# Kernel tuning notes

Hardware: AMD Instinct MI355X
Metric: run time of the kernel (lower is better)

## Reference

```python
import jax, jax.numpy as jnp
import numpy as np

B, N, D, H = 256, 256, 136, 128  # queries, docs/query, feature dim, hidden dim


def setup_inputs() -> dict:
    key = jax.random.key(0)
    ks = jax.random.split(key, 7)
    features = jax.random.uniform(ks[0], (B, N, D), dtype=jnp.float32)
    labels = jax.random.randint(ks[1], (B, N), 0, 5, dtype=jnp.int32)  # relevance grades 0..4
    # Small init scales keep MLP scores in (-1, 1) so log2(1 + max(s_i, s_j)) is well-defined
    W1 = jax.random.normal(ks[2], (D, H), dtype=jnp.float32) * 0.05
    b1 = jnp.zeros((H,), dtype=jnp.float32)
    W2 = jax.random.normal(ks[3], (H, H), dtype=jnp.float32) * 0.05
    b2 = jnp.zeros((H,), dtype=jnp.float32)
    W3 = jax.random.normal(ks[4], (H, 1), dtype=jnp.float32) * 0.02
    b3 = jnp.zeros((1,), dtype=jnp.float32)
    return {"features": features, "labels": labels,
            "W1": W1, "b1": b1, "W2": W2, "b2": b2, "W3": W3, "b3": b3}


def _scores(features, W1, b1, W2, b2, W3, b3):
    # Linear-ReLU-(Dropout: identity in eval)-Linear-ReLU-Linear, then squeeze(-1)
    h = jax.nn.relu(jnp.einsum('bnd,dh->bnh', features, W1) + b1)
    h = jax.nn.relu(jnp.einsum('bnh,hk->bnk', h, W2) + b2)
    return (jnp.einsum('bnh,ho->bno', h, W3) + b3).squeeze(-1)  # [B, N]


def _compute_lambdas(scores, labels):
    si = scores[:, :, None]        # s_i  [B, N, 1]
    sj = scores[:, None, :]        # s_j  [B, 1, N]
    li = labels[:, :, None]
    lj = labels[:, None, :]
    # lambda_ij = 0.5 * (1 - sigmoid(s_j - s_i)) = 0.5 * sigmoid(s_i - s_j)
    lam = 0.5 * jax.nn.sigmoid(si - sj)
    gain = jnp.exp2(labels.astype(scores.dtype))  # 2 ** l
    dndcg = jnp.abs((gain[:, :, None] - gain[:, None, :])
                    / (1.0 + jnp.log2(1.0 + jnp.maximum(si, sj))))
    A = jnp.where(li > lj, lam * dndcg, jnp.zeros((), scores.dtype))  # [B, N, N]
    # lambdas[i] += A[i, j] over j (pairs where l_i > l_j); lambdas[j] -= A[i, j]
    return A.sum(-1) - A.sum(-2)  # [B, N]


def reference(features, labels, W1, b1, W2, b2, W3, b3):
    scores = _scores(features, W1, b1, W2, b2, W3, b3)
    return _compute_lambdas(scores, labels)
```

## Files before the change

### kernel.cpp

```cpp
#include <hip/hip_runtime.h>
#include <hip/hip_bf16.h>

#define DIN  136
#define HH   128
#define NSEQ 256
#define NB   256
#define K1P  168

typedef __attribute__((ext_vector_type(4))) float f32x4;
typedef __attribute__((ext_vector_type(2))) float f32x2;
typedef __attribute__((ext_vector_type(8))) short bf16x8;

static __device__ __forceinline__ unsigned short f2bf(float f) {
    unsigned int u = __float_as_uint(f);
    u += 0x7fffu + ((u >> 16) & 1u);
    return (unsigned short)(u >> 16);
}

__global__ __launch_bounds__(256)
void prep_kernel(const float* __restrict__ W1, const float* __restrict__ W2,
                 short* __restrict__ w1t, short* __restrict__ w2t)
{
    const int nt = gridDim.x * 256;
    const int idx = blockIdx.x * 256 + threadIdx.x;
    for (int e = idx; e < HH * K1P; e += nt) {
        const int n = e / K1P, k = e - n * K1P;
        w1t[e] = (k < DIN) ? (short)f2bf(W1[k * HH + n]) : (short)0;
    }
    for (int e = idx; e < HH * HH; e += nt) {
        const int n = e >> 7, k = e & 127;
        w2t[e] = (short)f2bf(W2[k * HH + n]);
    }
}

__global__ __launch_bounds__(1024, 4)
void fused_kernel(const float* __restrict__ features,
                  const int*   __restrict__ labels,
                  const short* __restrict__ w1t,
                  const short* __restrict__ w2t,
                  const float* __restrict__ b1, const float* __restrict__ b2,
                  const float* __restrict__ W3, const float* __restrict__ b3,
                  float* __restrict__ out)
{
    __shared__ short  a_lds[NSEQ * K1P];
    __shared__ float4 sp[NSEQ];
    __shared__ float  s_part[4][NSEQ];

    const int t    = threadIdx.x;
    const int lane = t & 63;
    const int wv   = t >> 6;
    const int l15  = lane & 15;
    const int l4   = lane >> 4;
    const long row0 = (long)blockIdx.x * NSEQ;

    {
        const f32x2* src = (const f32x2*)(features + row0 * DIN);
        for (int i = t; i < NSEQ * DIN / 2; i += 1024) {
            f32x2 v = src[i];
            const int e = i * 2;
            const int r = e / DIN, k = e - r * DIN;
            *(unsigned int*)&a_lds[r * K1P + k] =
                (unsigned int)f2bf(v.x) | ((unsigned int)f2bf(v.y) << 16);
        }
        for (int i = t; i < NSEQ * 16; i += 1024) {
            const int r = i >> 4, k = DIN + (i & 15) * 2;
            *(unsigned int*)&a_lds[r * K1P + k] = 0u;
        }
    }
    __syncthreads();

    const int arow = (wv * 16 + l15) * K1P;

    f32x4 acc[8];
#pragma unroll
    for (int tn = 0; tn < 8; ++tn) {
        const float bv = b1[tn * 16 + l15];
        acc[tn] = (f32x4){bv, bv, bv, bv};
    }
    for (int kc = 0; kc < 5; ++kc) {
        const int kb = kc * 32 + l4 * 8;
        const bf16x8 afr = *(const bf16x8*)&a_lds[arow + kb];
        bf16x8 bfr[8];
#pragma unroll
        for (int tn = 0; tn < 8; ++tn)
            bfr[tn] = *(const bf16x8*)&w1t[(tn * 16 + l15) * K1P + kb];
#pragma unroll
        for (int tn = 0; tn < 8; ++tn)
            acc[tn] = __builtin_amdgcn_mfma_f32_16x16x32_bf16(afr, bfr[tn], acc[tn], 0, 0, 0);
    }

#pragma unroll
    for (int tn = 0; tn < 8; ++tn) {
        const int col = tn * 16 + l15;
#pragma unroll
        for (int j = 0; j < 4; ++j)
            a_lds[(wv * 16 + l4 * 4 + j) * K1P + col] =
                (short)f2bf(fmaxf(acc[tn][j], 0.f));
    }

    f32x4 acc2[8];
#pragma unroll
    for (int tn = 0; tn < 8; ++tn) {
        const float bv = b2[tn * 16 + l15];
        acc2[tn] = (f32x4){bv, bv, bv, bv};
    }
    for (int kc = 0; kc < 4; ++kc) {
        const int kb = kc * 32 + l4 * 8;
        const bf16x8 afr = *(const bf16x8*)&a_lds[arow + kb];
        bf16x8 bfr[8];
#pragma unroll
        for (int tn = 0; tn < 8; ++tn)
            bfr[tn] = *(const bf16x8*)&w2t[(tn * 16 + l15) * HH + kb];
#pragma unroll
        for (int tn = 0; tn < 8; ++tn)
            acc2[tn] = __builtin_amdgcn_mfma_f32_16x16x32_bf16(afr, bfr[tn], acc2[tn], 0, 0, 0);
    }

    {
        float w3v[8];
#pragma unroll
        for (int tn = 0; tn < 8; ++tn) w3v[tn] = W3[tn * 16 + l15];
        const float b3v = b3[0];
#pragma unroll
        for (int j = 0; j < 4; ++j) {
            float p = 0.f;
#pragma unroll
            for (int tn = 0; tn < 8; ++tn)
                p += fmaxf(acc2[tn][j], 0.f) * w3v[tn];
            p += __shfl_xor(p, 1, 64);
            p += __shfl_xor(p, 2, 64);
            p += __shfl_xor(p, 4, 64);
            p += __shfl_xor(p, 8, 64);
            if (l15 == 0) {
                const int row = wv * 16 + l4 * 4 + j;
                const float s = p + b3v;
                const int lab = labels[row0 + row];
                const float g = 0.5f * exp2f((float)lab);
                const float disc = 1.f / (1.f + log2f(1.f + s));
                sp[row] = make_float4(s * 1.44269504088896f,
                                      g, disc, 0.f);
            }
        }
    }
    __syncthreads();

    {
        const int i  = t & (NSEQ - 1);
        const int jg = t >> 8;
        const float4 me = sp[i];
        const float sci = me.x, gi = me.y, di = me.z;
        float accum = 0.f;
        const int j0 = jg * 64;
#pragma unroll 8
        for (int jj = 0; jj < 64; ++jj) {
            const float4 o = sp[j0 + jj];
            const float dg = o.y - gi;
            const float e  = exp2f(o.x - sci);
            const float r  = __builtin_amdgcn_rcpf(1.f + e);
            const float dmax = (sci > o.x) ? di : o.z;
            const float dn = fabsf(dg) * dmax;
            const float w  = (dg < 0.f) ? r : (r - 1.f);
            accum += dn * w;
        }
        s_part[jg][i] = accum;
    }
    __syncthreads();
    {
        const int i  = t & (NSEQ - 1);
        if ((t >> 8) == 0)
            out[row0 + i] = s_part[0][i] + s_part[1][i] +
                            s_part[2][i] + s_part[3][i];
    }
}

extern "C" void kernel_launch(void* const* d_in, const int* in_sizes, int n_in,
                              void* d_out, int out_size, void* d_ws, size_t ws_size,
                              hipStream_t stream)
{
    const float* features = (const float*)d_in[0];
    const int*   labels   = (const int*)d_in[1];
    const float* W1 = (const float*)d_in[2];
    const float* b1 = (const float*)d_in[3];
    const float* W2 = (const float*)d_in[4];
    const float* b2 = (const float*)d_in[5];
    const float* W3 = (const float*)d_in[6];
    const float* b3 = (const float*)d_in[7];

    short* w1t = (short*)d_ws;
    short* w2t = w1t + HH * K1P;
    float* out = (float*)d_out;

    prep_kernel<<<64, 256, 0, stream>>>(W1, W2, w1t, w2t);
    fused_kernel<<<NB, 1024, 0, stream>>>(
        features, labels, w1t, w2t, b1, b2, W3, b3, out);
}
```

Measured before the change: 121.8 us.

## Load features directly into MFMA A-fragments, shrink LDS, split B loads

Removes the LDS staging pass for the feature matrix: each lane now reads its fp32 feature row straight from global memory, converts it to bf16 and zeroes the padded K chunk in registers. The LDS buffer shrinks to a 136-stride hidden buffer that holds only layer-1 activations, and the launch bounds now ask for up to 8 waves per SIMD. The weight fragment loads are split into two halves of four to lower register pressure. In exchange, global reads become strided per row with less coalescing, and the row stride of 136 shorts may cause LDS bank conflicts.

```diff
diff --git a/kernel.cpp b/kernel.cpp
--- a/kernel.cpp
+++ b/kernel.cpp
@@ -6,9 +6,9 @@
 #define NSEQ 256
 #define NB   256
 #define K1P  168
+#define S2   136
 
 typedef __attribute__((ext_vector_type(4))) float f32x4;
-typedef __attribute__((ext_vector_type(2))) float f32x2;
 typedef __attribute__((ext_vector_type(8))) short bf16x8;
 
 static __device__ __forceinline__ unsigned short f2bf(float f) {
@@ -33,7 +33,7 @@
     }
 }
 
-__global__ __launch_bounds__(1024, 4)
+__global__ __launch_bounds__(1024, 8)
 void fused_kernel(const float* __restrict__ features,
                   const int*   __restrict__ labels,
                   const short* __restrict__ w1t,
@@ -42,7 +42,7 @@
                   const float* __restrict__ W3, const float* __restrict__ b3,
                   float* __restrict__ out)
 {
-    __shared__ short  a_lds[NSEQ * K1P];
+    __shared__ short  h1[NSEQ * S2];
     __shared__ float4 sp[NSEQ];
     __shared__ float  s_part[4][NSEQ];
 
@@ -53,23 +53,8 @@
     const int l4   = lane >> 4;
     const long row0 = (long)blockIdx.x * NSEQ;
 
-    {
-        const f32x2* src = (const f32x2*)(features + row0 * DIN);
-        for (int i = t; i < NSEQ * DIN / 2; i += 1024) {
-            f32x2 v = src[i];
-            const int e = i * 2;
-            const int r = e / DIN, k = e - r * DIN;
-            *(unsigned int*)&a_lds[r * K1P + k] =
-                (unsigned int)f2bf(v.x) | ((unsigned int)f2bf(v.y) << 16);
-        }
-        for (int i = t; i < NSEQ * 16; i += 1024) {
-            const int r = i >> 4, k = DIN + (i & 15) * 2;
-            *(unsigned int*)&a_lds[r * K1P + k] = 0u;
-        }
-    }
-    __syncthreads();
-
-    const int arow = (wv * 16 + l15) * K1P;
+    const float* frow = features + (row0 + wv * 16 + l15) * (long)DIN;
+    const int    arow = (wv * 16 + l15) * S2;
 
     f32x4 acc[8];
 #pragma unroll
@@ -79,14 +64,30 @@
     }
     for (int kc = 0; kc < 5; ++kc) {
         const int kb = kc * 32 + l4 * 8;
-        const bf16x8 afr = *(const bf16x8*)&a_lds[arow + kb];
-        bf16x8 bfr[8];
-#pragma unroll
-        for (int tn = 0; tn < 8; ++tn)
+        bf16x8 afr;
+        if (kb < DIN) {
+            const f32x4 g0 = *(const f32x4*)&frow[kb];
+            const f32x4 g1 = *(const f32x4*)&frow[kb + 4];
+            afr[0] = (short)f2bf(g0.x); afr[1] = (short)f2bf(g0.y);
+            afr[2] = (short)f2bf(g0.z); afr[3] = (short)f2bf(g0.w);
+            afr[4] = (short)f2bf(g1.x); afr[5] = (short)f2bf(g1.y);
+            afr[6] = (short)f2bf(g1.z); afr[7] = (short)f2bf(g1.w);
+        } else {
+            afr = (bf16x8){0,0,0,0,0,0,0,0};
+        }
+        bf16x8 bfr[4];
+#pragma unroll
+        for (int tn = 0; tn < 4; ++tn)
             bfr[tn] = *(const bf16x8*)&w1t[(tn * 16 + l15) * K1P + kb];
 #pragma unroll
-        for (int tn = 0; tn < 8; ++tn)
+        for (int tn = 0; tn < 4; ++tn)
             acc[tn] = __builtin_amdgcn_mfma_f32_16x16x32_bf16(afr, bfr[tn], acc[tn], 0, 0, 0);
+#pragma unroll
+        for (int tn = 0; tn < 4; ++tn)
+            bfr[tn] = *(const bf16x8*)&w1t[((tn + 4) * 16 + l15) * K1P + kb];
+#pragma unroll
+        for (int tn = 0; tn < 4; ++tn)
+            acc[tn + 4] = __builtin_amdgcn_mfma_f32_16x16x32_bf16(afr, bfr[tn], acc[tn + 4], 0, 0, 0);
     }
 
 #pragma unroll
@@ -94,7 +95,7 @@
         const int col = tn * 16 + l15;
 #pragma unroll
         for (int j = 0; j < 4; ++j)
-            a_lds[(wv * 16 + l4 * 4 + j) * K1P + col] =
+            h1[(wv * 16 + l4 * 4 + j) * S2 + col] =
                 (short)f2bf(fmaxf(acc[tn][j], 0.f));
     }
 
@@ -106,14 +107,20 @@
     }
     for (int kc = 0; kc < 4; ++kc) {
         const int kb = kc * 32 + l4 * 8;
-        const bf16x8 afr = *(const bf16x8*)&a_lds[arow + kb];
-        bf16x8 bfr[8];
-#pragma unroll
-        for (int tn = 0; tn < 8; ++tn)
+        const bf16x8 afr = *(const bf16x8*)&h1[arow + kb];
+        bf16x8 bfr[4];
+#pragma unroll
+        for (int tn = 0; tn < 4; ++tn)
             bfr[tn] = *(const bf16x8*)&w2t[(tn * 16 + l15) * HH + kb];
 #pragma unroll
-        for (int tn = 0; tn < 8; ++tn)
+        for (int tn = 0; tn < 4; ++tn)
             acc2[tn] = __builtin_amdgcn_mfma_f32_16x16x32_bf16(afr, bfr[tn], acc2[tn], 0, 0, 0);
+#pragma unroll
+        for (int tn = 0; tn < 4; ++tn)
+            bfr[tn] = *(const bf16x8*)&w2t[((tn + 4) * 16 + l15) * HH + kb];
+#pragma unroll
+        for (int tn = 0; tn < 4; ++tn)
+            acc2[tn + 4] = __builtin_amdgcn_mfma_f32_16x16x32_bf16(afr, bfr[tn], acc2[tn + 4], 0, 0, 0);
     }
 
     {
@@ -166,7 +173,7 @@
     }
     __syncthreads();
     {
-        const int i  = t & (NSEQ - 1);
+        const int i = t & (NSEQ - 1);
         if ((t >> 8) == 0)
             out[row0 + i] = s_part[0][i] + s_part[1][i] +
                             s_part[2][i] + s_part[3][i];
```

Measured after the change: 125.5 us. 1.03x slower.

## Stage bf16 weights in LDS, shrink row stride, vectorize feature conversion

Applied to the files above, without the earlier changes.

Both bf16 weight matrices are now copied into shared memory once per block and the MFMA B-fragments are read from there instead of from global memory. The row stride drops from 168 to 136, which removes the zero-padding writes. The tail K chunk (128..135) becomes a masked MFMA where only lanes with l4==0 load data. Feature loads are widened to float4 and packed with hardware bf16x2 conversion. LDS use grows to about 136KB with aliased regions, so an extra barrier is added, and occupancy is limited to one block per CU.

```diff
diff --git a/kernel.cpp b/kernel.cpp
--- a/kernel.cpp
+++ b/kernel.cpp
@@ -5,46 +5,51 @@
 #define HH   128
 #define NSEQ 256
 #define NB   256
-#define K1P  168
+#define ST   136
 
 typedef __attribute__((ext_vector_type(4))) float f32x4;
-typedef __attribute__((ext_vector_type(2))) float f32x2;
 typedef __attribute__((ext_vector_type(8))) short bf16x8;
 
-static __device__ __forceinline__ unsigned short f2bf(float f) {
-    unsigned int u = __float_as_uint(f);
-    u += 0x7fffu + ((u >> 16) & 1u);
-    return (unsigned short)(u >> 16);
+static __device__ __forceinline__ unsigned cvt2(float lo, float hi) {
+    __hip_bfloat162 h = __float22bfloat162_rn(make_float2(lo, hi));
+    return *(unsigned*)&h;
+}
+static __device__ __forceinline__ short f2bf1(float f) {
+    __hip_bfloat16 h = __float2bfloat16(f);
+    return *(short*)&h;
 }
 
 __global__ __launch_bounds__(256)
 void prep_kernel(const float* __restrict__ W1, const float* __restrict__ W2,
-                 short* __restrict__ w1t, short* __restrict__ w2t)
+                 short* __restrict__ w1s, short* __restrict__ w2s)
 {
     const int nt = gridDim.x * 256;
     const int idx = blockIdx.x * 256 + threadIdx.x;
-    for (int e = idx; e < HH * K1P; e += nt) {
-        const int n = e / K1P, k = e - n * K1P;
-        w1t[e] = (k < DIN) ? (short)f2bf(W1[k * HH + n]) : (short)0;
-    }
-    for (int e = idx; e < HH * HH; e += nt) {
-        const int n = e >> 7, k = e & 127;
-        w2t[e] = (short)f2bf(W2[k * HH + n]);
+    for (int e = idx; e < HH * ST; e += nt) {
+        const int n = e / ST, k = e - n * ST;
+        w1s[e] = f2bf1(W1[k * HH + n]);
+    }
+    for (int e = idx; e < HH * ST; e += nt) {
+        const int n = e / ST, k = e - n * ST;
+        w2s[e] = (k < HH) ? f2bf1(W2[k * HH + n]) : (short)0;
     }
 }
 
 __global__ __launch_bounds__(1024, 4)
 void fused_kernel(const float* __restrict__ features,
                   const int*   __restrict__ labels,
-                  const short* __restrict__ w1t,
-                  const short* __restrict__ w2t,
+                  const short* __restrict__ w1s,
+                  const short* __restrict__ w2s,
                   const float* __restrict__ b1, const float* __restrict__ b2,
                   const float* __restrict__ W3, const float* __restrict__ b3,
                   float* __restrict__ out)
 {
-    __shared__ short  a_lds[NSEQ * K1P];
-    __shared__ float4 sp[NSEQ];
-    __shared__ float  s_part[4][NSEQ];
+    __shared__ __align__(16) char smem[139264];
+    short* a_lds  = (short*)smem;
+    short* w1_lds = (short*)(smem + 69632);
+    short* w2_lds = (short*)(smem + 104448);
+    float4* sp    = (float4*)smem;
+    float (*s_part)[NSEQ] = (float (*)[NSEQ])(smem + 4096);
 
     const int t    = threadIdx.x;
     const int lane = t & 63;
@@ -54,55 +59,31 @@
     const long row0 = (long)blockIdx.x * NSEQ;
 
     {
-        const f32x2* src = (const f32x2*)(features + row0 * DIN);
-        for (int i = t; i < NSEQ * DIN / 2; i += 1024) {
-            f32x2 v = src[i];
-            const int e = i * 2;
-            const int r = e / DIN, k = e - r * DIN;
-            *(unsigned int*)&a_lds[r * K1P + k] =
-                (unsigned int)f2bf(v.x) | ((unsigned int)f2bf(v.y) << 16);
-        }
-        for (int i = t; i < NSEQ * 16; i += 1024) {
-            const int r = i >> 4, k = DIN + (i & 15) * 2;
-            *(unsigned int*)&a_lds[r * K1P + k] = 0u;
-        }
-    }
-    __syncthreads();
-
-    const int arow = (wv * 16 + l15) * K1P;
+        const uint4* src = (const uint4*)w1s;
+        uint4* dst = (uint4*)w1_lds;
+        for (int i = t; i < 2 * HH * ST / 8; i += 1024)
+            dst[i] = src[i];
+    }
+    {
+        const f32x4* src = (const f32x4*)(features + row0 * DIN);
+        for (int i = t; i < NSEQ * DIN / 4; i += 1024) {
+            const f32x4 v = src[i];
+            const int r = i / 34, c = i - r * 34;
+            uint2 p;
+            p.x = cvt2(v.x, v.y);
+            p.y = cvt2(v.z, v.w);
+            *(uint2*)&a_lds[r * ST + c * 4] = p;
+        }
+    }
+    __syncthreads();
+
+    const int arow = (wv * 16 + l15) * ST;
 
     f32x4 acc[8];
 #pragma unroll
     for (int tn = 0; tn < 8; ++tn) {
         const float bv = b1[tn * 16 + l15];
         acc[tn] = (f32x4){bv, bv, bv, bv};
-    }
-    for (int kc = 0; kc < 5; ++kc) {
-        const int kb = kc * 32 + l4 * 8;
-        const bf16x8 afr = *(const bf16x8*)&a_lds[arow + kb];
-        bf16x8 bfr[8];
-#pragma unroll
-        for (int tn = 0; tn < 8; ++tn)
-            bfr[tn] = *(const bf16x8*)&w1t[(tn * 16 + l15) * K1P + kb];
-#pragma unroll
-        for (int tn = 0; tn < 8; ++tn)
-            acc[tn] = __builtin_amdgcn_mfma_f32_16x16x32_bf16(afr, bfr[tn], acc[tn], 0, 0, 0);
-    }
-
-#pragma unroll
-    for (int tn = 0; tn < 8; ++tn) {
-        const int col = tn * 16 + l15;
-#pragma unroll
-        for (int j = 0; j < 4; ++j)
-            a_lds[(wv * 16 + l4 * 4 + j) * K1P + col] =
-                (short)f2bf(fmaxf(acc[tn][j], 0.f));
-    }
-
-    f32x4 acc2[8];
-#pragma unroll
-    for (int tn = 0; tn < 8; ++tn) {
-        const float bv = b2[tn * 16 + l15];
-        acc2[tn] = (f32x4){bv, bv, bv, bv};
     }
     for (int kc = 0; kc < 4; ++kc) {
         const int kb = kc * 32 + l4 * 8;
@@ -110,11 +91,53 @@
         bf16x8 bfr[8];
 #pragma unroll
         for (int tn = 0; tn < 8; ++tn)
-            bfr[tn] = *(const bf16x8*)&w2t[(tn * 16 + l15) * HH + kb];
+            bfr[tn] = *(const bf16x8*)&w1_lds[(tn * 16 + l15) * ST + kb];
+#pragma unroll
+        for (int tn = 0; tn < 8; ++tn)
+            acc[tn] = __builtin_amdgcn_mfma_f32_16x16x32_bf16(afr, bfr[tn], acc[tn], 0, 0, 0);
+    }
+    {
+        bf16x8 afr = (bf16x8){0,0,0,0,0,0,0,0};
+        bf16x8 bfr[8];
+#pragma unroll
+        for (int tn = 0; tn < 8; ++tn) bfr[tn] = (bf16x8){0,0,0,0,0,0,0,0};
+        if (l4 == 0) {
+            afr = *(const bf16x8*)&a_lds[arow + 128];
+#pragma unroll
+            for (int tn = 0; tn < 8; ++tn)
+                bfr[tn] = *(const bf16x8*)&w1_lds[(tn * 16 + l15) * ST + 128];
+        }
+#pragma unroll
+        for (int tn = 0; tn < 8; ++tn)
+            acc[tn] = __builtin_amdgcn_mfma_f32_16x16x32_bf16(afr, bfr[tn], acc[tn], 0, 0, 0);
+    }
+
+#pragma unroll
+    for (int tn = 0; tn < 8; ++tn) {
+        const int col = tn * 16 + l15;
+#pragma unroll
+        for (int j = 0; j < 4; ++j)
+            a_lds[(wv * 16 + l4 * 4 + j) * ST + col] = f2bf1(fmaxf(acc[tn][j], 0.f));
+    }
+
+    f32x4 acc2[8];
+#pragma unroll
+    for (int tn = 0; tn < 8; ++tn) {
+        const float bv = b2[tn * 16 + l15];
+        acc2[tn] = (f32x4){bv, bv, bv, bv};
+    }
+    for (int kc = 0; kc < 4; ++kc) {
+        const int kb = kc * 32 + l4 * 8;
+        const bf16x8 afr = *(const bf16x8*)&a_lds[arow + kb];
+        bf16x8 bfr[8];
+#pragma unroll
+        for (int tn = 0; tn < 8; ++tn)
+            bfr[tn] = *(const bf16x8*)&w2_lds[(tn * 16 + l15) * ST + kb];
 #pragma unroll
         for (int tn = 0; tn < 8; ++tn)
             acc2[tn] = __builtin_amdgcn_mfma_f32_16x16x32_bf16(afr, bfr[tn], acc2[tn], 0, 0, 0);
     }
+    __syncthreads();
 
     {
         float w3v[8];
@@ -166,7 +189,7 @@
     }
     __syncthreads();
     {
-        const int i  = t & (NSEQ - 1);
+        const int i = t & (NSEQ - 1);
         if ((t >> 8) == 0)
             out[row0 + i] = s_part[0][i] + s_part[1][i] +
                             s_part[2][i] + s_part[3][i];
@@ -186,11 +209,11 @@
     const float* W3 = (const float*)d_in[6];
     const float* b3 = (const float*)d_in[7];
 
-    short* w1t = (short*)d_ws;
-    short* w2t = w1t + HH * K1P;
+    short* w1s = (short*)d_ws;
+    short* w2s = w1s + HH * ST;
     float* out = (float*)d_out;
 
-    prep_kernel<<<64, 256, 0, stream>>>(W1, W2, w1t, w2t);
+    prep_kernel<<<64, 256, 0, stream>>>(W1, W2, w1s, w2s);
     fused_kernel<<<NB, 1024, 0, stream>>>(
-        features, labels, w1t, w2t, b1, b2, W3, b3, out);
-}
+        features, labels, w1s, w2s, b1, b2, W3, b3, out);
+}
```

After: 106.0 us. 1.15x faster.

## Stage pre-swizzled weights in LDS, stream features to registers, split queries across blocks

Applied to the files above, without the earlier changes.

Weights are pre-packed into MFMA fragment order and copied once into LDS. Features are loaded straight from global into B-operand registers, and the layer-1 output is passed to layer 2 through lane shuffles instead of an LDS round trip. The grid doubles to 512 blocks of 512 threads. Each block recomputes the full 256-row MLP for its query and does only half of the pairwise lambda rows, with a swizzled block-to-query mapping. This trades redundant MLP work for better occupancy and fewer LDS transfers.

```diff
diff --git a/kernel.cpp b/kernel.cpp
--- a/kernel.cpp
+++ b/kernel.cpp
@@ -5,148 +5,176 @@
 #define HH   128
 #define NSEQ 256
 #define NB   256
-#define K1P  168
+
+#define W1F_SH (8 * 5 * 64 * 8)
+#define W2F_SH (8 * 4 * 64 * 8)
 
 typedef __attribute__((ext_vector_type(4))) float f32x4;
-typedef __attribute__((ext_vector_type(2))) float f32x2;
 typedef __attribute__((ext_vector_type(8))) short bf16x8;
 
-static __device__ __forceinline__ unsigned short f2bf(float f) {
-    unsigned int u = __float_as_uint(f);
-    u += 0x7fffu + ((u >> 16) & 1u);
-    return (unsigned short)(u >> 16);
+static __device__ __forceinline__ unsigned cvt2(float lo, float hi) {
+    __hip_bfloat162 h = __float22bfloat162_rn(make_float2(lo, hi));
+    return *(unsigned*)&h;
+}
+static __device__ __forceinline__ short f2bf1(float f) {
+    __hip_bfloat16 h = __float2bfloat16(f);
+    return *(short*)&h;
 }
 
 __global__ __launch_bounds__(256)
 void prep_kernel(const float* __restrict__ W1, const float* __restrict__ W2,
-                 short* __restrict__ w1t, short* __restrict__ w2t)
+                 short* __restrict__ w1f, short* __restrict__ w2f)
 {
     const int nt = gridDim.x * 256;
     const int idx = blockIdx.x * 256 + threadIdx.x;
-    for (int e = idx; e < HH * K1P; e += nt) {
-        const int n = e / K1P, k = e - n * K1P;
-        w1t[e] = (k < DIN) ? (short)f2bf(W1[k * HH + n]) : (short)0;
-    }
-    for (int e = idx; e < HH * HH; e += nt) {
-        const int n = e >> 7, k = e & 127;
-        w2t[e] = (short)f2bf(W2[k * HH + n]);
-    }
-}
-
-__global__ __launch_bounds__(1024, 4)
+    for (int e = idx; e < W1F_SH; e += nt) {
+        const int tn = e / 2560, r = e - tn * 2560;
+        const int kc = r >> 9, r2 = r & 511, l = r2 >> 3, j = r2 & 7;
+        const int n = tn * 16 + (l & 15);
+        const int k = kc * 32 + (l >> 4) * 8 + j;
+        w1f[e] = (k < DIN) ? f2bf1(W1[k * HH + n]) : (short)0;
+    }
+    for (int e = idx; e < W2F_SH; e += nt) {
+        const int tn = e >> 11, r = e & 2047;
+        const int kc = r >> 9, r2 = r & 511, l = r2 >> 3, j = r2 & 7;
+        const int n = tn * 16 + (l & 15);
+        const int k = kc * 32 + (l >> 4) * 8 + j;
+        w2f[e] = f2bf1(W2[k * HH + n]);
+    }
+}
+
+__global__ __launch_bounds__(512, 4)
 void fused_kernel(const float* __restrict__ features,
                   const int*   __restrict__ labels,
-                  const short* __restrict__ w1t,
-                  const short* __restrict__ w2t,
+                  const short* __restrict__ w1f,
                   const float* __restrict__ b1, const float* __restrict__ b2,
                   const float* __restrict__ W3, const float* __restrict__ b3,
                   float* __restrict__ out)
 {
-    __shared__ short  a_lds[NSEQ * K1P];
-    __shared__ float4 sp[NSEQ];
-    __shared__ float  s_part[4][NSEQ];
+    __shared__ __align__(16) char smem[79872];
+    short* w1_lds = (short*)smem;
+    short* w2_lds = (short*)(smem + 40960);
+    float4* sp    = (float4*)(smem + 73728);
+    float (*s_part)[128] = (float (*)[128])(smem + 77824);
 
     const int t    = threadIdx.x;
     const int lane = t & 63;
-    const int wv   = t >> 6;
+    const int wave = t >> 6;
     const int l15  = lane & 15;
-    const int l4   = lane >> 4;
-    const long row0 = (long)blockIdx.x * NSEQ;
+    const int kg2  = lane >> 4;
+
+    const int bid     = blockIdx.x;
+    const int logical = (bid >> 3) + (bid & 7) * 64;
+    const int q       = logical >> 1;
+    const int ih      = (logical & 1) * 128;
+    const long row0   = (long)q * NSEQ;
 
     {
-        const f32x2* src = (const f32x2*)(features + row0 * DIN);
-        for (int i = t; i < NSEQ * DIN / 2; i += 1024) {
-            f32x2 v = src[i];
-            const int e = i * 2;
-            const int r = e / DIN, k = e - r * DIN;
-            *(unsigned int*)&a_lds[r * K1P + k] =
-                (unsigned int)f2bf(v.x) | ((unsigned int)f2bf(v.y) << 16);
-        }
-        for (int i = t; i < NSEQ * 16; i += 1024) {
-            const int r = i >> 4, k = DIN + (i & 15) * 2;
-            *(unsigned int*)&a_lds[r * K1P + k] = 0u;
-        }
+        const uint4* src = (const uint4*)w1f;
+        uint4* dst = (uint4*)smem;
+#pragma unroll
+        for (int m = 0; m < 9; ++m) dst[t + m * 512] = src[t + m * 512];
     }
     __syncthreads();
 
-    const int arow = (wv * 16 + l15) * K1P;
-
-    f32x4 acc[8];
-#pragma unroll
-    for (int tn = 0; tn < 8; ++tn) {
-        const float bv = b1[tn * 16 + l15];
-        acc[tn] = (f32x4){bv, bv, bv, bv};
-    }
-    for (int kc = 0; kc < 5; ++kc) {
-        const int kb = kc * 32 + l4 * 8;
-        const bf16x8 afr = *(const bf16x8*)&a_lds[arow + kb];
-        bf16x8 bfr[8];
+    const float log2e = 1.44269504088896f;
+    const float b3v = b3[0];
+
+    for (int mt = 0; mt < 2; ++mt) {
+        const float* frow =
+            features + (row0 + mt * 128 + wave * 16 + l15) * (long)DIN;
+
+        f32x4 acc1[8];
 #pragma unroll
         for (int tn = 0; tn < 8; ++tn)
-            bfr[tn] = *(const bf16x8*)&w1t[(tn * 16 + l15) * K1P + kb];
+#pragma unroll
+            for (int qq = 0; qq < 4; ++qq)
+                acc1[tn][qq] = b1[tn * 16 + kg2 * 4 + qq];
+#pragma unroll
+        for (int kc = 0; kc < 5; ++kc) {
+            bf16x8 bfr;
+            if (kc < 4 || kg2 == 0) {
+                const float* fp = frow + kc * 32 + kg2 * 8;
+                const f32x4 g0 = *(const f32x4*)fp;
+                const f32x4 g1 = *(const f32x4*)(fp + 4);
+                union { bf16x8 v; unsigned u[4]; } bb;
+                bb.u[0] = cvt2(g0.x, g0.y); bb.u[1] = cvt2(g0.z, g0.w);
+                bb.u[2] = cvt2(g1.x, g1.y); bb.u[3] = cvt2(g1.z, g1.w);
+                bfr = bb.v;
+            } else {
+                bfr = (bf16x8){0,0,0,0,0,0,0,0};
+            }
+#pragma unroll
+            for (int tn = 0; tn < 8; ++tn) {
+                const bf16x8 afr =
+                    *(const bf16x8*)&w1_lds[((tn * 5 + kc) * 64 + lane) * 8];
+                acc1[tn] = __builtin_amdgcn_mfma_f32_16x16x32_bf16(
+                    afr, bfr, acc1[tn], 0, 0, 0);
+            }
+        }
+
+        unsigned p[16];
+#pragma unroll
+        for (int tn = 0; tn < 8; ++tn) {
+            p[tn * 2 + 0] = cvt2(fmaxf(acc1[tn][0], 0.f), fmaxf(acc1[tn][1], 0.f));
+            p[tn * 2 + 1] = cvt2(fmaxf(acc1[tn][2], 0.f), fmaxf(acc1[tn][3], 0.f));
+        }
+
+        f32x4 acc2[8];
 #pragma unroll
         for (int tn = 0; tn < 8; ++tn)
-            acc[tn] = __builtin_amdgcn_mfma_f32_16x16x32_bf16(afr, bfr[tn], acc[tn], 0, 0, 0);
-    }
-
-#pragma unroll
-    for (int tn = 0; tn < 8; ++tn) {
-        const int col = tn * 16 + l15;
-#pragma unroll
-        for (int j = 0; j < 4; ++j)
-            a_lds[(wv * 16 + l4 * 4 + j) * K1P + col] =
-                (short)f2bf(fmaxf(acc[tn][j], 0.f));
-    }
-
-    f32x4 acc2[8];
-#pragma unroll
-    for (int tn = 0; tn < 8; ++tn) {
-        const float bv = b2[tn * 16 + l15];
-        acc2[tn] = (f32x4){bv, bv, bv, bv};
-    }
-    for (int kc = 0; kc < 4; ++kc) {
-        const int kb = kc * 32 + l4 * 8;
-        const bf16x8 afr = *(const bf16x8*)&a_lds[arow + kb];
-        bf16x8 bfr[8];
+#pragma unroll
+            for (int qq = 0; qq < 4; ++qq)
+                acc2[tn][qq] = b2[tn * 16 + kg2 * 4 + qq];
+        const int s0 = l15 + 32 * (kg2 & 1);
+        const int s1 = s0 + 16;
+        const bool hiTn = (kg2 >> 1) & 1;
+#pragma unroll
+        for (int kc = 0; kc < 4; ++kc) {
+            const unsigned a0 = __shfl((int)p[4 * kc + 0], s0);
+            const unsigned c0 = __shfl((int)p[4 * kc + 2], s0);
+            const unsigned a1 = __shfl((int)p[4 * kc + 1], s0);
+            const unsigned c1 = __shfl((int)p[4 * kc + 3], s0);
+            const unsigned a2 = __shfl((int)p[4 * kc + 0], s1);
+            const unsigned c2 = __shfl((int)p[4 * kc + 2], s1);
+            const unsigned a3 = __shfl((int)p[4 * kc + 1], s1);
+            const unsigned c3 = __shfl((int)p[4 * kc + 3], s1);
+            union { bf16x8 v; unsigned u[4]; } bb;
+            bb.u[0] = hiTn ? c0 : a0;
+            bb.u[1] = hiTn ? c1 : a1;
+            bb.u[2] = hiTn ? c2 : a2;
+            bb.u[3] = hiTn ? c3 : a3;
+#pragma unroll
+            for (int tn = 0; tn < 8; ++tn) {
+                const bf16x8 afr =
+                    *(const bf16x8*)&w2_lds[((tn * 4 + kc) * 64 + lane) * 8];
+                acc2[tn] = __builtin_amdgcn_mfma_f32_16x16x32_bf16(
+                    afr, bb.v, acc2[tn], 0, 0, 0);
+            }
+        }
+
+        float partial = 0.f;
 #pragma unroll
         for (int tn = 0; tn < 8; ++tn)
-            bfr[tn] = *(const bf16x8*)&w2t[(tn * 16 + l15) * HH + kb];
-#pragma unroll
-        for (int tn = 0; tn < 8; ++tn)
-            acc2[tn] = __builtin_amdgcn_mfma_f32_16x16x32_bf16(afr, bfr[tn], acc2[tn], 0, 0, 0);
-    }
+#pragma unroll
+            for (int qq = 0; qq < 4; ++qq)
+                partial += fmaxf(acc2[tn][qq], 0.f) * W3[tn * 16 + kg2 * 4 + qq];
+        partial += __shfl_xor(partial, 16, 64);
+        partial += __shfl_xor(partial, 32, 64);
+        if (lane < 16) {
+            const int row = mt * 128 + wave * 16 + lane;
+            const float s = partial + b3v;
+            const int lab = labels[row0 + row];
+            const float g = 0.5f * exp2f((float)lab);
+            const float disc = 1.f / (1.f + log2f(1.f + s));
+            sp[row] = make_float4(s * log2e, g, disc, 0.f);
+        }
+    }
+    __syncthreads();
 
     {
-        float w3v[8];
-#pragma unroll
-        for (int tn = 0; tn < 8; ++tn) w3v[tn] = W3[tn * 16 + l15];
-        const float b3v = b3[0];
-#pragma unroll
-        for (int j = 0; j < 4; ++j) {
-            float p = 0.f;
-#pragma unroll
-            for (int tn = 0; tn < 8; ++tn)
-                p += fmaxf(acc2[tn][j], 0.f) * w3v[tn];
-            p += __shfl_xor(p, 1, 64);
-            p += __shfl_xor(p, 2, 64);
-            p += __shfl_xor(p, 4, 64);
-            p += __shfl_xor(p, 8, 64);
-            if (l15 == 0) {
-                const int row = wv * 16 + l4 * 4 + j;
-                const float s = p + b3v;
-                const int lab = labels[row0 + row];
-                const float g = 0.5f * exp2f((float)lab);
-                const float disc = 1.f / (1.f + log2f(1.f + s));
-                sp[row] = make_float4(s * 1.44269504088896f,
-                                      g, disc, 0.f);
-            }
-        }
-    }
-    __syncthreads();
-
-    {
-        const int i  = t & (NSEQ - 1);
-        const int jg = t >> 8;
+        const int i  = ih + (t & 127);
+        const int jg = t >> 7;
         const float4 me = sp[i];
         const float sci = me.x, gi = me.y, di = me.z;
         float accum = 0.f;
@@ -162,15 +190,12 @@
             const float w  = (dg < 0.f) ? r : (r - 1.f);
             accum += dn * w;
         }
-        s_part[jg][i] = accum;
+        s_part[jg][t & 127] = accum;
     }
     __syncthreads();
-    {
-        const int i  = t & (NSEQ - 1);
-        if ((t >> 8) == 0)
-            out[row0 + i] = s_part[0][i] + s_part[1][i] +
-                            s_part[2][i] + s_part[3][i];
-    }
+    if (t < 128)
+        out[row0 + ih + t] = s_part[0][t] + s_part[1][t] +
+                             s_part[2][t] + s_part[3][t];
 }
 
 extern "C" void kernel_launch(void* const* d_in, const int* in_sizes, int n_in,
@@ -186,11 +211,11 @@
     const float* W3 = (const float*)d_in[6];
     const float* b3 = (const float*)d_in[7];
 
-    short* w1t = (short*)d_ws;
-    short* w2t = w1t + HH * K1P;
+    short* w1f = (short*)d_ws;
+    short* w2f = w1f + W1F_SH;
     float* out = (float*)d_out;
 
-    prep_kernel<<<64, 256, 0, stream>>>(W1, W2, w1t, w2t);
-    fused_kernel<<<NB, 1024, 0, stream>>>(
-        features, labels, w1t, w2t, b1, b2, W3, b3, out);
-}
+    prep_kernel<<<64, 256, 0, stream>>>(W1, W2, w1f, w2f);
+    fused_kernel<<<NB * 2, 512, 0, stream>>>(
+        features, labels, w1f, b1, b2, W3, b3, out);
+}
```

Measured after the change: 334.6 us. 2.75x slower.
